# Optimization experiments

Hardware: AMD Instinct MI355X
Metric: run time of the kernel (lower is better)

## Reference

```python
import jax, jax.numpy as jnp
import numpy as np

B, T, C, H = 4, 2048, 1024, 16
D = C // H  # head dim = 64

def setup_inputs() -> dict:
    key = jax.random.key(0)
    k1, k2, k3 = jax.random.split(key, 3)
    x = jax.random.normal(k1, (B, T, C), dtype=jnp.float32)
    # torch Linear weight [out,in]; store transposed for x @ W
    W_attn = jax.random.normal(k2, (C, 3 * C), dtype=jnp.float32) * (1.0 / np.sqrt(C))
    W_proj = jax.random.normal(k3, (C, C), dtype=jnp.float32) * (1.0 / np.sqrt(C))
    return {"x": x, "W_attn": W_attn, "W_proj": W_proj}

def reference(x, W_attn, W_proj):
    qkv = x @ W_attn                          # [B,T,3C]
    q, k, v = jnp.split(qkv, 3, axis=-1)
    # [B,T,C] -> [B,H,T,D]
    def heads(t):
        return t.reshape(B, T, H, D).transpose(0, 2, 1, 3)
    q, k, v = heads(q), heads(k), heads(v)
    att = jnp.einsum('bhqd,bhkd->bhqk', q, k) * (1.0 / np.sqrt(D))  # [B,H,T,T]
    causal = jnp.tril(jnp.ones((T, T), dtype=bool))
    att = jnp.where(causal[None, None, :, :], att, -jnp.inf)
    att = jax.nn.softmax(att, axis=-1)
    y = jnp.einsum('bhqk,bhkd->bhqd', att, v)  # [B,H,T,D]
    y = y.transpose(0, 2, 1, 3).reshape(B, T, C)
    return y @ W_proj
```

## Files before the change

kernel.cpp:

```cpp
#include <hip/hip_runtime.h>
#include <hip/hip_bf16.h>

#define BB 4
#define TT 2048
#define CC 1024
#define HH 16
#define DD 64
#define MM (BB*TT)

typedef unsigned short u16;
typedef __bf16 bf16x8 __attribute__((ext_vector_type(8)));
typedef __bf16 bf16x4v __attribute__((ext_vector_type(4)));
typedef u16 u16x8 __attribute__((ext_vector_type(8)));
typedef u16 u16x4 __attribute__((ext_vector_type(4)));
typedef float f32x4 __attribute__((ext_vector_type(4)));

__device__ __forceinline__ u16 f2bf(float f) {
  union { float f; unsigned u; } v; v.f = f;
  unsigned u = v.u;
  return (u16)((u + 0x7fffu + ((u >> 16) & 1u)) >> 16);
}
__device__ __forceinline__ float bf2f(u16 s) {
  union { unsigned u; float f; } v; v.u = ((unsigned)s) << 16; return v.f;
}
__device__ __forceinline__ bf16x8 ld_bf16x8(const u16* p) {
  return *reinterpret_cast<const bf16x8*>(p);
}
__device__ __forceinline__ f32x4 zero4() {
  f32x4 z; z[0] = 0.f; z[1] = 0.f; z[2] = 0.f; z[3] = 0.f; return z;
}

__device__ __forceinline__ void gld_lds16(const u16* g, u16* l) {
  __builtin_amdgcn_global_load_lds(
      (const __attribute__((address_space(1))) void*)g,
      (__attribute__((address_space(3))) void*)l, 16, 0, 0);
}
__device__ __forceinline__ void wait_vm0() { __builtin_amdgcn_s_waitcnt(0x0F70); }

__device__ __forceinline__ float lane_pull(float x, int srclane) {
  int r = __builtin_amdgcn_ds_bpermute(srclane << 2, __builtin_bit_cast(int, x));
  return __builtin_bit_cast(float, r);
}

#define NC4B ((MM * CC / 4) / 256)
__global__ void k_prep(const float* __restrict__ x, u16* __restrict__ xb,
                       const float* __restrict__ Wa, u16* __restrict__ Wab,
                       const float* __restrict__ Wp, u16* __restrict__ Wpb) {
  __shared__ float tile[32][33];
  const int bx = blockIdx.x;
  if (bx < NC4B) {
    int i = bx * 256 + threadIdx.x;
    const float4 v = reinterpret_cast<const float4*>(x)[i];
    u16x4 r; r.x = f2bf(v.x); r.y = f2bf(v.y); r.z = f2bf(v.z); r.w = f2bf(v.w);
    reinterpret_cast<u16x4*>(xb)[i] = r;
    return;
  }
  const float* W; u16* Wt; int K, N, b2;
  if (bx < NC4B + 3072) { W = Wa; Wt = Wab; K = CC; N = 3 * CC; b2 = bx - NC4B; }
  else                  { W = Wp; Wt = Wpb; K = CC; N = CC;     b2 = bx - NC4B - 3072; }
  const int nblk = N / 32;
  const int nb = (b2 % nblk) * 32, kb = (b2 / nblk) * 32;
  const int tx = threadIdx.x & 31, ty = threadIdx.x >> 5;
  #pragma unroll
  for (int i = ty; i < 32; i += 8)
    tile[i][tx] = W[(size_t)(kb + i) * N + nb + tx];
  __syncthreads();
  #pragma unroll
  for (int i = ty; i < 32; i += 8)
    Wt[(size_t)(nb + i) * K + kb + tx] = f2bf(tile[tx][i]);
}

template<int EPI>
__global__ __launch_bounds__(256, 3)
void k_gemm_bt(const u16* __restrict__ A, const u16* __restrict__ Bt,
               float* __restrict__ outF, u16* __restrict__ qb, u16* __restrict__ kb,
               u16* __restrict__ vt, int N, int K)
{
  __shared__ u16 As[128 * 64];
  __shared__ u16 Bs[128 * 64];
  const int tid  = threadIdx.x;
  const int lane = tid & 63, w = tid >> 6;
  const int l16  = lane & 15, quad = lane >> 4;
  const int wr = w >> 1, wc = w & 1;
  const int m0 = blockIdx.y * 128, n0 = blockIdx.x * 128;
  const int lr8 = lane >> 3, lc8 = lane & 7;

  f32x4 acc[4][4];
  #pragma unroll
  for (int i = 0; i < 4; ++i)
    #pragma unroll
    for (int j = 0; j < 4; ++j) acc[i][j] = zero4();

  for (int k0 = 0; k0 < K; k0 += 64) {
    __syncthreads();
    #pragma unroll
    for (int p = 0; p < 4; ++p) {
      const int row = w * 32 + p * 8 + lr8;
      const int cs  = lc8 ^ (row & 7);
      gld_lds16(A  + (size_t)(m0 + row) * K + k0 + cs * 8, &As[(w * 32 + p * 8) * 64]);
      gld_lds16(Bt + (size_t)(n0 + row) * K + k0 + cs * 8, &Bs[(w * 32 + p * 8) * 64]);
    }
    wait_vm0();
    __syncthreads();
    #pragma unroll
    for (int s = 0; s < 2; ++s) {
      bf16x8 af[4], bfr[4];
      #pragma unroll
      for (int i = 0; i < 4; ++i) {
        int mrow = wr * 64 + i * 16 + l16;
        af[i]  = ld_bf16x8(&As[mrow * 64 + ((s * 4 + quad) ^ (l16 & 7)) * 8]);
        int nrow = wc * 64 + i * 16 + l16;
        bfr[i] = ld_bf16x8(&Bs[nrow * 64 + ((s * 4 + quad) ^ (l16 & 7)) * 8]);
      }
      #pragma unroll
      for (int i = 0; i < 4; ++i)
        #pragma unroll
        for (int j = 0; j < 4; ++j)
          acc[i][j] = __builtin_amdgcn_mfma_f32_16x16x32_bf16(af[i], bfr[j], acc[i][j], 0, 0, 0);
    }
  }

  #pragma unroll
  for (int i = 0; i < 4; ++i) {
    #pragma unroll
    for (int j = 0; j < 4; ++j) {
      const int n = n0 + wc * 64 + j * 16 + l16;
      const int mb = m0 + wr * 64 + i * 16 + quad * 4;
      if (EPI == 0) {
        #pragma unroll
        for (int r = 0; r < 4; ++r)
          outF[(size_t)(mb + r) * N + n] = acc[i][j][r];
      } else {
        const int b = mb >> 11, tb = mb & 2047;
        if (n < CC) {
          const int h = n >> 6, d = n & 63;
          #pragma unroll
          for (int r = 0; r < 4; ++r)
            qb[(((size_t)(b * HH + h) * TT + tb + r) << 6) + d] = f2bf(acc[i][j][r]);
        } else if (n < 2 * CC) {
          const int n2 = n - CC; const int h = n2 >> 6, d = n2 & 63;
          #pragma unroll
          for (int r = 0; r < 4; ++r)
            kb[(((size_t)(b * HH + h) * TT + tb + r) << 6) + d] = f2bf(acc[i][j][r]);
        } else {
          const int n2 = n - 2 * CC; const int h = n2 >> 6, d = n2 & 63;
          u16x4 cv;
          #pragma unroll
          for (int r = 0; r < 4; ++r) cv[r] = f2bf(acc[i][j][r]);
          *reinterpret_cast<u16x4*>(
              vt + ((size_t)(b * HH + h) * DD + d) * TT + tb) = cv;
        }
      }
    }
  }
}

__global__ __launch_bounds__(256, 4)
void k_attn(const u16* __restrict__ qb, const u16* __restrict__ kb,
            const u16* __restrict__ vt, u16* __restrict__ y)
{
  __shared__ u16 Ks[128 * 64];
  __shared__ u16 Vs[64 * 128];
  __shared__ u16 QP[64 * 64];
  const int tid  = threadIdx.x;
  const int lane = tid & 63, w = tid >> 6;
  const int l16  = lane & 15, quad = lane >> 4;
  const int lr8 = lane >> 3, lc8 = lane & 7;

  const int bx = blockIdx.x;
  const int qt = 31 - (bx >> 6);
  const int bh = bx & 63;
  const int h  = bh & 15, b = bh >> 4;

  const u16* qptr = qb + ((size_t)bh * TT + qt * 64) * DD;
  const u16* kptr = kb + (size_t)bh * TT * DD;
  const u16* vptr = vt + (size_t)bh * DD * TT;

  const float qscale = 0.125f * 1.44269504088896340736f;
  #pragma unroll
  for (int p = 0; p < 2; ++p) {
    const int r = w * 16 + p * 8 + lr8;
    u16x8 v = *reinterpret_cast<const u16x8*>(qptr + (size_t)r * DD + lc8 * 8);
    u16x8 o;
    #pragma unroll
    for (int e = 0; e < 8; ++e) o[e] = f2bf(bf2f(v[e]) * qscale);
    *reinterpret_cast<u16x8*>(&QP[r * 64 + (lc8 ^ lr8) * 8]) = o;
  }
  bf16x8 qf[2];
  #pragma unroll
  for (int s = 0; s < 2; ++s)
    qf[s] = ld_bf16x8(&QP[(w * 16 + l16) * 64 + ((s * 4 + quad) ^ (l16 & 7)) * 8]);

  float rsum = 0.f;
  f32x4 O[4];
  #pragma unroll
  for (int j = 0; j < 4; ++j) O[j] = zero4();

  const int qend = qt * 64;
  const int nkt  = (qt >> 1) + 1;
  for (int kt = 0; kt < nkt; ++kt) {
    __syncthreads();
    {
      const u16* kt0 = kptr + (size_t)kt * 128 * DD;
      #pragma unroll
      for (int p = 0; p < 4; ++p) {
        const int row = w * 32 + p * 8 + lr8;
        const int cs  = lc8 ^ (row & 7);
        gld_lds16(kt0 + (size_t)row * DD + cs * 8, &Ks[(w * 32 + p * 8) * 64]);
      }
      #pragma unroll
      for (int p = 0; p < 4; ++p) {
        const int d  = w * 16 + p * 4 + (lane >> 4);
        const int cs = (lane & 15) ^ (d & 7);
        gld_lds16(vptr + (size_t)d * TT + kt * 128 + cs * 8,
                  &Vs[(w * 16 + p * 4) * 128]);
      }
    }
    wait_vm0();
    __syncthreads();

    #pragma unroll
    for (int h2 = 0; h2 < 2; ++h2) {
      const int k0 = kt * 128 + h2 * 64;
      if (k0 <= qend) {
        f32x4 St[4];
        #pragma unroll
        for (int j = 0; j < 4; ++j) St[j] = zero4();
        #pragma unroll
        for (int s = 0; s < 2; ++s) {
          #pragma unroll
          for (int j = 0; j < 4; ++j) {
            bf16x8 kfr = ld_bf16x8(&Ks[(h2 * 64 + j * 16 + l16) * 64 +
                                       ((s * 4 + quad) ^ (l16 & 7)) * 8]);
            St[j] = __builtin_amdgcn_mfma_f32_16x16x32_bf16(kfr, qf[s], St[j], 0, 0, 0);
          }
        }
        if (k0 == qend) {
          const int qg = w * 16 + l16;
          #pragma unroll
          for (int j = 0; j < 4; ++j)
            #pragma unroll
            for (int r = 0; r < 4; ++r)
              if (j * 16 + quad * 4 + r > qg) St[j][r] = -__builtin_inff();
        }

        #pragma unroll
        for (int j = 0; j < 4; ++j)
          #pragma unroll
          for (int r = 0; r < 4; ++r) {
            float p = __builtin_amdgcn_exp2f(St[j][r]);
            St[j][r] = p;
            rsum += p;
          }

        #pragma unroll
        for (int j = 0; j < 4; ++j) {
          union { bf16x4v bv; u16x4 u; } cv;
          cv.bv[0] = (__bf16)St[j][0]; cv.bv[1] = (__bf16)St[j][1];
          cv.bv[2] = (__bf16)St[j][2]; cv.bv[3] = (__bf16)St[j][3];
          const int c = j * 2 + (quad >> 1);
          const int off = w * 1024 + l16 * 64 + ((c ^ (l16 & 7)) << 3) + ((quad & 1) << 2);
          *reinterpret_cast<u16x4*>(&QP[off]) = cv.u;
        }
        #pragma unroll
        for (int s = 0; s < 2; ++s) {
          bf16x8 pf = ld_bf16x8(&QP[w * 1024 + l16 * 64 +
                                    ((s * 4 + quad) ^ (l16 & 7)) * 8]);
          #pragma unroll
          for (int j = 0; j < 4; ++j) {
            bf16x8 vf = ld_bf16x8(&Vs[(j * 16 + l16) * 128 +
                                      ((h2 * 8 + s * 4 + quad) ^ (l16 & 7)) * 8]);
            O[j] = __builtin_amdgcn_mfma_f32_16x16x32_bf16(pf, vf, O[j], 0, 0, 0);
          }
        }
      }
    }
  }

  rsum += __shfl_xor(rsum, 16);
  rsum += __shfl_xor(rsum, 32);
  const float linv = 1.0f / rsum;
  f32x4 lv;
  #pragma unroll
  for (int r = 0; r < 4; ++r) lv[r] = lane_pull(linv, quad * 4 + r);
  #pragma unroll
  for (int j = 0; j < 4; ++j) {
    O[j] *= lv;
    #pragma unroll
    for (int r = 0; r < 4; ++r) {
      int t  = qt * 64 + w * 16 + quad * 4 + r;
      int ch = h * 64 + j * 16 + l16;
      y[(size_t)(b * TT + t) * CC + ch] = f2bf(O[j][r]);
    }
  }
}

extern "C" void kernel_launch(void* const* d_in, const int* in_sizes, int n_in,
                              void* d_out, int out_size, void* d_ws, size_t ws_size,
                              hipStream_t stream) {
  const float* x  = (const float*)d_in[0];
  const float* Wa = (const float*)d_in[1];
  const float* Wp = (const float*)d_in[2];
  float* out = (float*)d_out;

  u16* ws   = (u16*)d_ws;
  u16* xb   = ws;
  u16* Wab  = xb   + (size_t)MM * CC;
  u16* Wpb  = Wab  + (size_t)3 * CC * CC;
  u16* qbuf = Wpb  + (size_t)CC * CC;
  u16* kbuf = qbuf + (size_t)MM * CC;
  u16* vtb  = kbuf + (size_t)MM * CC;
  u16* yb   = vtb  + (size_t)MM * CC;

  k_prep<<<NC4B + 3072 + 1024, 256, 0, stream>>>(x, xb, Wa, Wab, Wp, Wpb);
  k_gemm_bt<1><<<dim3(3 * CC / 128, MM / 128), 256, 0, stream>>>(
      xb, Wab, nullptr, qbuf, kbuf, vtb, 3 * CC, CC);
  k_attn<<<64 * 32, 256, 0, stream>>>(qbuf, kbuf, vtb, yb);
  k_gemm_bt<0><<<dim3(CC / 128, MM / 128), 256, 0, stream>>>(
      yb, Wpb, out, nullptr, nullptr, nullptr, CC, CC);
}
```

Baseline: 231.2 us.

## Pipeline attention K tiles with double buffering and overlap V loads

Shrinks the attention KV tile from 128 to 64 keys and double-buffers K in shared memory, prefetching the next K tile while the current tile's QK^T and softmax run. V for the current tile is loaded at the start of the iteration and waited on only before the PV MFMA, using a partial vmcnt wait. The smaller LDS footprint also allows launch bounds of 5 blocks per CU. In exchange there are more loop iterations and two barriers per tile.

```diff
diff --git a/kernel.cpp b/kernel.cpp
--- a/kernel.cpp
+++ b/kernel.cpp
@@ -36,6 +36,7 @@
       (__attribute__((address_space(3))) void*)l, 16, 0, 0);
 }
 __device__ __forceinline__ void wait_vm0() { __builtin_amdgcn_s_waitcnt(0x0F70); }
+__device__ __forceinline__ void wait_vm2() { __builtin_amdgcn_s_waitcnt(0x0F72); }
 
 __device__ __forceinline__ float lane_pull(float x, int srclane) {
   int r = __builtin_amdgcn_ds_bpermute(srclane << 2, __builtin_bit_cast(int, x));
@@ -155,12 +156,12 @@
   }
 }
 
-__global__ __launch_bounds__(256, 4)
+__global__ __launch_bounds__(256, 5)
 void k_attn(const u16* __restrict__ qb, const u16* __restrict__ kb,
             const u16* __restrict__ vt, u16* __restrict__ y)
 {
-  __shared__ u16 Ks[128 * 64];
-  __shared__ u16 Vs[64 * 128];
+  __shared__ u16 Ks[2][64 * 64];
+  __shared__ u16 Vs[64 * 64];
   __shared__ u16 QP[64 * 64];
   const int tid  = threadIdx.x;
   const int lane = tid & 63, w = tid >> 6;
@@ -176,6 +177,11 @@
   const u16* kptr = kb + (size_t)bh * TT * DD;
   const u16* vptr = vt + (size_t)bh * DD * TT;
 
+  #pragma unroll
+  for (int p = 0; p < 2; ++p) {
+    const int row = w * 16 + p * 8 + lr8;
+    gld_lds16(kptr + (size_t)row * DD + (lc8 ^ lr8) * 8, &Ks[0][(w * 16 + p * 8) * 64]);
+  }
   const float qscale = 0.125f * 1.44269504088896340736f;
   #pragma unroll
   for (int p = 0; p < 2; ++p) {
@@ -196,83 +202,81 @@
   #pragma unroll
   for (int j = 0; j < 4; ++j) O[j] = zero4();
 
-  const int qend = qt * 64;
-  const int nkt  = (qt >> 1) + 1;
-  for (int kt = 0; kt < nkt; ++kt) {
-    __syncthreads();
-    {
-      const u16* kt0 = kptr + (size_t)kt * 128 * DD;
-      #pragma unroll
-      for (int p = 0; p < 4; ++p) {
-        const int row = w * 32 + p * 8 + lr8;
-        const int cs  = lc8 ^ (row & 7);
-        gld_lds16(kt0 + (size_t)row * DD + cs * 8, &Ks[(w * 32 + p * 8) * 64]);
-      }
-      #pragma unroll
-      for (int p = 0; p < 4; ++p) {
-        const int d  = w * 16 + p * 4 + (lane >> 4);
-        const int cs = (lane & 15) ^ (d & 7);
-        gld_lds16(vptr + (size_t)d * TT + kt * 128 + cs * 8,
-                  &Vs[(w * 16 + p * 4) * 128]);
-      }
-    }
+  const int ktiles = qt + 1;
+  for (int kt = 0; kt < ktiles; ++kt) {
+    const int buf = kt & 1;
     wait_vm0();
     __syncthreads();
 
     #pragma unroll
-    for (int h2 = 0; h2 < 2; ++h2) {
-      const int k0 = kt * 128 + h2 * 64;
-      if (k0 <= qend) {
-        f32x4 St[4];
+    for (int p = 0; p < 2; ++p) {
+      const int row = w * 16 + p * 8 + lr8;
+      gld_lds16(vptr + (size_t)row * TT + kt * 64 + (lc8 ^ lr8) * 8,
+                &Vs[(w * 16 + p * 8) * 64]);
+    }
+    const bool pre = (kt + 1 < ktiles);
+    if (pre) {
+      const u16* kt0 = kptr + (size_t)(kt + 1) * 64 * DD;
+      #pragma unroll
+      for (int p = 0; p < 2; ++p) {
+        const int row = w * 16 + p * 8 + lr8;
+        gld_lds16(kt0 + (size_t)row * DD + (lc8 ^ lr8) * 8,
+                  &Ks[buf ^ 1][(w * 16 + p * 8) * 64]);
+      }
+    }
+
+    f32x4 St[4];
+    #pragma unroll
+    for (int j = 0; j < 4; ++j) St[j] = zero4();
+    #pragma unroll
+    for (int s = 0; s < 2; ++s) {
+      #pragma unroll
+      for (int j = 0; j < 4; ++j) {
+        bf16x8 kfr = ld_bf16x8(&Ks[buf][(j * 16 + l16) * 64 +
+                                        ((s * 4 + quad) ^ (l16 & 7)) * 8]);
+        St[j] = __builtin_amdgcn_mfma_f32_16x16x32_bf16(kfr, qf[s], St[j], 0, 0, 0);
+      }
+    }
+    if (kt == qt) {
+      const int qg = w * 16 + l16;
+      #pragma unroll
+      for (int j = 0; j < 4; ++j)
         #pragma unroll
-        for (int j = 0; j < 4; ++j) St[j] = zero4();
-        #pragma unroll
-        for (int s = 0; s < 2; ++s) {
-          #pragma unroll
-          for (int j = 0; j < 4; ++j) {
-            bf16x8 kfr = ld_bf16x8(&Ks[(h2 * 64 + j * 16 + l16) * 64 +
-                                       ((s * 4 + quad) ^ (l16 & 7)) * 8]);
-            St[j] = __builtin_amdgcn_mfma_f32_16x16x32_bf16(kfr, qf[s], St[j], 0, 0, 0);
-          }
-        }
-        if (k0 == qend) {
-          const int qg = w * 16 + l16;
-          #pragma unroll
-          for (int j = 0; j < 4; ++j)
-            #pragma unroll
-            for (int r = 0; r < 4; ++r)
-              if (j * 16 + quad * 4 + r > qg) St[j][r] = -__builtin_inff();
-        }
-
-        #pragma unroll
-        for (int j = 0; j < 4; ++j)
-          #pragma unroll
-          for (int r = 0; r < 4; ++r) {
-            float p = __builtin_amdgcn_exp2f(St[j][r]);
-            St[j][r] = p;
-            rsum += p;
-          }
-
-        #pragma unroll
-        for (int j = 0; j < 4; ++j) {
-          union { bf16x4v bv; u16x4 u; } cv;
-          cv.bv[0] = (__bf16)St[j][0]; cv.bv[1] = (__bf16)St[j][1];
-          cv.bv[2] = (__bf16)St[j][2]; cv.bv[3] = (__bf16)St[j][3];
-          const int c = j * 2 + (quad >> 1);
-          const int off = w * 1024 + l16 * 64 + ((c ^ (l16 & 7)) << 3) + ((quad & 1) << 2);
-          *reinterpret_cast<u16x4*>(&QP[off]) = cv.u;
-        }
-        #pragma unroll
-        for (int s = 0; s < 2; ++s) {
-          bf16x8 pf = ld_bf16x8(&QP[w * 1024 + l16 * 64 +
-                                    ((s * 4 + quad) ^ (l16 & 7)) * 8]);
-          #pragma unroll
-          for (int j = 0; j < 4; ++j) {
-            bf16x8 vf = ld_bf16x8(&Vs[(j * 16 + l16) * 128 +
-                                      ((h2 * 8 + s * 4 + quad) ^ (l16 & 7)) * 8]);
-            O[j] = __builtin_amdgcn_mfma_f32_16x16x32_bf16(pf, vf, O[j], 0, 0, 0);
-          }
-        }
+        for (int r = 0; r < 4; ++r)
+          if (j * 16 + quad * 4 + r > qg) St[j][r] = -__builtin_inff();
+    }
+
+    #pragma unroll
+    for (int j = 0; j < 4; ++j)
+      #pragma unroll
+      for (int r = 0; r < 4; ++r) {
+        float p = __builtin_amdgcn_exp2f(St[j][r]);
+        St[j][r] = p;
+        rsum += p;
+      }
+
+    #pragma unroll
+    for (int j = 0; j < 4; ++j) {
+      union { bf16x4v bv; u16x4 u; } cv;
+      cv.bv[0] = (__bf16)St[j][0]; cv.bv[1] = (__bf16)St[j][1];
+      cv.bv[2] = (__bf16)St[j][2]; cv.bv[3] = (__bf16)St[j][3];
+      const int c = j * 2 + (quad >> 1);
+      const int off = w * 1024 + l16 * 64 + ((c ^ (l16 & 7)) << 3) + ((quad & 1) << 2);
+      *reinterpret_cast<u16x4*>(&QP[off]) = cv.u;
+    }
+
+    if (pre) wait_vm2(); else wait_vm0();
+    __syncthreads();
+
+    #pragma unroll
+    for (int s = 0; s < 2; ++s) {
+      bf16x8 pf = ld_bf16x8(&QP[w * 1024 + l16 * 64 +
+                                ((s * 4 + quad) ^ (l16 & 7)) * 8]);
+      #pragma unroll
+      for (int j = 0; j < 4; ++j) {
+        bf16x8 vf = ld_bf16x8(&Vs[(j * 16 + l16) * 64 +
+                                  ((s * 4 + quad) ^ (l16 & 7)) * 8]);
+        O[j] = __builtin_amdgcn_mfma_f32_16x16x32_bf16(pf, vf, O[j], 0, 0, 0);
       }
     }
   }
```

Result: slower. 241.7 us (+4.6%).
